# Kernel tuning notes

Measured on AMD Instinct MI355X. Metric: run time of the kernel, lower is better.

Reference implementation:

```python
import jax, jax.numpy as jnp
import numpy as np

B, C, H, W = 4, 256, 64, 64
DQ = C // 8

def setup_inputs() -> dict:
    key = jax.random.key(0)
    ks = jax.random.split(key, 7)
    x = jax.random.normal(ks[0], (B, C, H, W), dtype=jnp.float32)
    # 1x1 convs == per-pixel linear layers: weight [out, in], bias [out]
    Wq = jax.random.normal(ks[1], (DQ, C), dtype=jnp.float32) * (1.0 / np.sqrt(C))
    bq = jax.random.normal(ks[2], (DQ,), dtype=jnp.float32) * 0.01
    Wk = jax.random.normal(ks[3], (DQ, C), dtype=jnp.float32) * (1.0 / np.sqrt(C))
    bk = jax.random.normal(ks[4], (DQ,), dtype=jnp.float32) * 0.01
    Wv = jax.random.normal(ks[5], (C, C), dtype=jnp.float32) * (1.0 / np.sqrt(C))
    bv = jax.random.normal(ks[6], (C,), dtype=jnp.float32) * 0.01
    return {"x": x, "Wq": Wq, "bq": bq, "Wk": Wk, "bk": bk, "Wv": Wv, "bv": bv}

def reference(x, Wq, bq, Wk, bk, Wv, bv):
    b, c, h, w = x.shape
    n = h * w
    xf = x.reshape(b, c, n)                                  # [b,c,n]
    Q = jnp.einsum('dc,bcn->bnd', Wq, xf) + bq               # [b,n,dq]
    K = jnp.einsum('dc,bcn->bdn', Wk, xf) + bk[None, :, None]  # [b,dq,n]
    A = jax.nn.softmax(jnp.einsum('bnd,bdm->bnm', Q, K), axis=-1)  # [b,n,n]
    V = jnp.einsum('oc,bcn->bon', Wv, xf) + bv[None, :, None]      # [b,c,n]
    # torch: bmm(V, A^T) -> out[b,c,i] = sum_j V[b,c,j] * A[b,i,j]
    out = jnp.einsum('bcj,bij->bci', V, A)
    return x + out.reshape(b, c, h, w)
```

## Files before the change

kernel.cpp:

```cpp
#include <hip/hip_runtime.h>
#include <math.h>

#define BB 4
#define CC 256
#define NN 4096
#define DQ 32
#define LOG2E 1.44269504f

typedef _Float16 half8 __attribute__((ext_vector_type(8)));
typedef _Float16 half4 __attribute__((ext_vector_type(4)));
typedef float float4v __attribute__((ext_vector_type(4)));

__global__ __launch_bounds__(64) void prep_kernel(
    const float* __restrict__ Wq, const float* __restrict__ bq,
    const float* __restrict__ Wk, const float* __restrict__ bk,
    const float* __restrict__ Wv, const float* __restrict__ bv,
    _Float16* __restrict__ Wh, float* __restrict__ bh)
{
    int o = blockIdx.x, t = threadIdx.x;
    const float* src; float scale = 1.0f, bias;
    if (o < DQ)            { src = Wq + o * CC;        scale = LOG2E; bias = bq[o] * LOG2E; }
    else if (o < 2 * DQ)   { src = Wk + (o - DQ) * CC;                bias = bk[o - DQ]; }
    else                   { src = Wv + (o - 2 * DQ) * CC;            bias = bv[o - 2 * DQ]; }
    float4 v = *(const float4*)(src + t * 4);
    half4 h = { (_Float16)(v.x * scale), (_Float16)(v.y * scale),
                (_Float16)(v.z * scale), (_Float16)(v.w * scale) };
    *(half4*)(Wh + o * CC + t * 4) = h;
    if (t == 0) bh[o] = bias;
}

__global__ __launch_bounds__(256) void proj_kernel(
    const float* __restrict__ x, const _Float16* __restrict__ Wh,
    const float* __restrict__ bh,
    _Float16* __restrict__ Qt, _Float16* __restrict__ Kt,
    _Float16* __restrict__ Vh)
{
    __shared__ _Float16 xl[64 * 256];
    __shared__ _Float16 os_qk[64 * 72];
    __shared__ _Float16 os_v[256 * 72];

    const int tid = threadIdx.x;
    const int lane = tid & 63, w = tid >> 6;
    const int i16 = lane & 15, q = lane >> 4;
    const int n0 = blockIdx.x * 64, b = blockIdx.y;

    const float* xb = x + (size_t)b * CC * NN + n0;
    #pragma unroll
    for (int u = 0; u < 16; ++u) {
        int idx = u * 256 + tid;
        int c = idx >> 4, n4 = idx & 15;
        float4 v = *(const float4*)(xb + (size_t)c * NN + n4 * 4);
        int chunk = c >> 3, cl = c & 7;
        float vv[4] = {v.x, v.y, v.z, v.w};
        #pragma unroll
        for (int e = 0; e < 4; ++e) {
            int n = n4 * 4 + e;
            xl[n * 256 + ((chunk ^ (n & 31)) * 8) + cl] = (_Float16)vv[e];
        }
    }

    float4v acc[5][4];
    const int obase = 80 * w;
    #pragma unroll
    for (int ot = 0; ot < 5; ++ot) {
        float4 b4 = *(const float4*)(bh + obase + 16 * ot + 4 * q);
        #pragma unroll
        for (int nt = 0; nt < 4; ++nt)
            acc[ot][nt] = (float4v){b4.x, b4.y, b4.z, b4.w};
    }
    __syncthreads();

    #pragma unroll
    for (int k = 0; k < 8; ++k) {
        half8 af[5], bf[4];
        #pragma unroll
        for (int ot = 0; ot < 5; ++ot)
            af[ot] = *(const half8*)(Wh + (size_t)(obase + 16 * ot + i16) * CC + k * 32 + 8 * q);
        #pragma unroll
        for (int nt = 0; nt < 4; ++nt) {
            int n = 16 * nt + i16;
            bf[nt] = *(const half8*)&xl[n * 256 + (((4 * k + q) ^ (n & 31)) * 8)];
        }
        #pragma unroll
        for (int ot = 0; ot < 5; ++ot)
            #pragma unroll
            for (int nt = 0; nt < 4; ++nt)
                acc[ot][nt] = __builtin_amdgcn_mfma_f32_16x16x32_f16(af[ot], bf[nt], acc[ot][nt], 0, 0, 0);
    }

    #pragma unroll
    for (int ot = 0; ot < 5; ++ot) {
        int og = obase + 16 * ot;
        #pragma unroll
        for (int nt = 0; nt < 4; ++nt) {
            int n = 16 * nt + i16;
            if (og < 64) {
                half4 hv = { (_Float16)acc[ot][nt][0], (_Float16)acc[ot][nt][1],
                             (_Float16)acc[ot][nt][2], (_Float16)acc[ot][nt][3] };
                *(half4*)&os_qk[n * 72 + og + 4 * q] = hv;
            } else {
                int cb = og - 64 + 4 * q;
                #pragma unroll
                for (int r = 0; r < 4; ++r)
                    os_v[(cb + r) * 72 + n] = (_Float16)acc[ot][nt][r];
            }
        }
    }
    __syncthreads();

    _Float16* Qtb = Qt + (size_t)b * NN * DQ;
    _Float16* Ktb = Kt + (size_t)b * NN * DQ;
    #pragma unroll
    for (int u = 0; u < 2; ++u) {
        int ct = u * 256 + tid;
        int n = ct >> 3, p = ct & 7;
        half8 hv = *(const half8*)&os_qk[n * 72 + 8 * p];
        if (p < 4) *(half8*)(Qtb + (size_t)(n0 + n) * DQ + 8 * p) = hv;
        else       *(half8*)(Ktb + (size_t)(n0 + n) * DQ + 8 * (p - 4)) = hv;
    }
    _Float16* Vb = Vh + (size_t)b * CC * NN;
    #pragma unroll
    for (int u = 0; u < 8; ++u) {
        int c = u * 32 + (tid >> 3), p = tid & 7;
        half8 hv = *(const half8*)&os_v[c * 72 + 8 * p];
        *(half8*)(Vb + (size_t)c * NN + n0 + 8 * p) = hv;
    }
}

__global__ __launch_bounds__(256) void rowstat_kernel(
    const _Float16* __restrict__ Qt, const _Float16* __restrict__ Kt,
    float* __restrict__ M2, float* __restrict__ L)
{
    __shared__ _Float16 k_lds[64 * 32];
    const int tid = threadIdx.x;
    const int lane = tid & 63, w = tid >> 6;
    const int i16 = lane & 15, q = lane >> 4;
    const int q0 = blockIdx.x * 64, js = blockIdx.y, b = blockIdx.z;

    const _Float16* Qtb = Qt + (size_t)b * NN * DQ;
    const _Float16* Ktb = Kt + (size_t)b * NN * DQ;
    half8 qb = *(const half8*)(Qtb + (size_t)(q0 + 16 * w + i16) * DQ + 8 * q);

    float m = -INFINITY, l = 0.f;
    for (int j0 = js * 2048; j0 < (js + 1) * 2048; j0 += 64) {
        __syncthreads();
        {
            int j = tid >> 2, dg = tid & 3;
            half8 kv = *(const half8*)(Ktb + (size_t)(j0 + j) * DQ + 8 * dg);
            *(half8*)&k_lds[j * 32 + ((dg ^ (j & 3)) * 8)] = kv;
        }
        __syncthreads();
        float4v s[4];
        #pragma unroll
        for (int jt = 0; jt < 4; ++jt) {
            int j = 16 * jt + i16;
            half8 ka = *(const half8*)&k_lds[j * 32 + ((q ^ (j & 3)) * 8)];
            float4v z = {0.f, 0.f, 0.f, 0.f};
            s[jt] = __builtin_amdgcn_mfma_f32_16x16x32_f16(ka, qb, z, 0, 0, 0);
        }
        float tmax = s[0][0];
        #pragma unroll
        for (int jt = 0; jt < 4; ++jt)
            #pragma unroll
            for (int r = 0; r < 4; ++r)
                tmax = fmaxf(tmax, s[jt][r]);
        float mnew = fmaxf(m, tmax);
        float sum = 0.f;
        #pragma unroll
        for (int jt = 0; jt < 4; ++jt)
            #pragma unroll
            for (int r = 0; r < 4; ++r)
                sum += exp2f(s[jt][r] - mnew);
        l = l * exp2f(m - mnew) + sum;
        m = mnew;
    }
    #pragma unroll
    for (int off = 16; off <= 32; off <<= 1) {
        float mo = __shfl_xor(m, off, 64);
        float lo = __shfl_xor(l, off, 64);
        float mn = fmaxf(m, mo);
        l = l * exp2f(m - mn) + lo * exp2f(mo - mn);
        m = mn;
    }
    if (q == 0) {
        int qi = q0 + 16 * w + i16;
        M2[((size_t)b * 2 + js) * NN + qi] = m;
        L[((size_t)b * 2 + js) * NN + qi] = l;
    }
}

__global__ __launch_bounds__(256) void attn_kernel(
    const float* __restrict__ x,
    const _Float16* __restrict__ Qt, const _Float16* __restrict__ Kt,
    const _Float16* __restrict__ Vh,
    const float* __restrict__ M2, const float* __restrict__ L,
    float* __restrict__ out)
{
    __shared__ _Float16 k_lds[64 * 32];
    __shared__ _Float16 v_lds[256 * 64];
    __shared__ _Float16 ps[32 * 72];

    const int tid = threadIdx.x;
    const int w = tid >> 6, lane = tid & 63;
    const int i16 = lane & 15, q = lane >> 4;
    const int i0 = blockIdx.x * 32, b = blockIdx.y;

    const _Float16* Ktb = Kt + (size_t)b * NN * DQ;
    const _Float16* Vb  = Vh + (size_t)b * CC * NN;

    float m2v[2], linv[2];
    #pragma unroll
    for (int it = 0; it < 2; ++it) {
        int qi = i0 + 16 * it + i16;
        float m0 = M2[((size_t)b * 2 + 0) * NN + qi];
        float m1 = M2[((size_t)b * 2 + 1) * NN + qi];
        float l0 = L[((size_t)b * 2 + 0) * NN + qi];
        float l1 = L[((size_t)b * 2 + 1) * NN + qi];
        float mm = fmaxf(m0, m1);
        float ll = l0 * exp2f(m0 - mm) + l1 * exp2f(m1 - mm);
        m2v[it] = mm;
        linv[it] = 1.0f / ll;
    }

    half8 qb[2];
    {
        const _Float16* Qtb = Qt + (size_t)b * NN * DQ;
        qb[0] = *(const half8*)(Qtb + (size_t)(i0 + i16) * DQ + 8 * q);
        qb[1] = *(const half8*)(Qtb + (size_t)(i0 + 16 + i16) * DQ + 8 * q);
    }

    float4v O[4][2];
    #pragma unroll
    for (int ct = 0; ct < 4; ++ct)
        #pragma unroll
        for (int it = 0; it < 2; ++it)
            O[ct][it] = (float4v){0.f, 0.f, 0.f, 0.f};

    for (int j0 = 0; j0 < NN; j0 += 64) {
        __syncthreads();
        {
            int j = tid >> 2, dg = tid & 3;
            half8 kv = *(const half8*)(Ktb + (size_t)(j0 + j) * DQ + 8 * dg);
            *(half8*)&k_lds[j * 32 + ((dg ^ (j & 3)) * 8)] = kv;
        }
        {
            int cb = tid >> 3, jg = tid & 7;
            #pragma unroll
            for (int u = 0; u < 8; ++u) {
                int c = u * 32 + cb;
                half8 vv = *(const half8*)(Vb + (size_t)c * NN + j0 + jg * 8);
                *(half8*)&v_lds[c * 64 + ((jg ^ (c & 7)) * 8)] = vv;
            }
        }
        __syncthreads();

        {
            int j = 16 * w + i16;
            half8 ka = *(const half8*)&k_lds[j * 32 + ((q ^ (j & 3)) * 8)];
            #pragma unroll
            for (int it = 0; it < 2; ++it) {
                float4v z = {0.f, 0.f, 0.f, 0.f};
                float4v s = __builtin_amdgcn_mfma_f32_16x16x32_f16(ka, qb[it], z, 0, 0, 0);
                half4 hv = { (_Float16)exp2f(s[0] - m2v[it]),
                             (_Float16)exp2f(s[1] - m2v[it]),
                             (_Float16)exp2f(s[2] - m2v[it]),
                             (_Float16)exp2f(s[3] - m2v[it]) };
                *(half4*)&ps[(16 * it + i16) * 72 + 16 * w + 4 * q] = hv;
            }
        }
        __syncthreads();

        half8 pb[2][2];
        #pragma unroll
        for (int ks = 0; ks < 2; ++ks)
            #pragma unroll
            for (int it = 0; it < 2; ++it)
                pb[ks][it] = *(const half8*)&ps[(16 * it + i16) * 72 + 32 * ks + 8 * q];
        #pragma unroll
        for (int ct = 0; ct < 4; ++ct) {
            int c = 64 * w + 16 * ct + i16;
            #pragma unroll
            for (int ks = 0; ks < 2; ++ks) {
                int g = 4 * ks + q;
                half8 va = *(const half8*)&v_lds[c * 64 + ((g ^ (c & 7)) * 8)];
                #pragma unroll
                for (int it = 0; it < 2; ++it)
                    O[ct][it] = __builtin_amdgcn_mfma_f32_16x16x32_f16(va, pb[ks][it], O[ct][it], 0, 0, 0);
            }
        }
    }

    const float* xb = x + (size_t)b * CC * NN;
    float* ob = out + (size_t)b * CC * NN;
    #pragma unroll
    for (int ct = 0; ct < 4; ++ct)
        #pragma unroll
        for (int it = 0; it < 2; ++it)
            #pragma unroll
            for (int r = 0; r < 4; ++r) {
                int c = 64 * w + 16 * ct + 4 * q + r;
                size_t idx = (size_t)c * NN + i0 + 16 * it + i16;
                ob[idx] = xb[idx] + O[ct][it][r] * linv[it];
            }
}

extern "C" void kernel_launch(void* const* d_in, const int* in_sizes, int n_in,
                              void* d_out, int out_size, void* d_ws, size_t ws_size,
                              hipStream_t stream) {
    const float* x  = (const float*)d_in[0];
    const float* Wq = (const float*)d_in[1];
    const float* bq = (const float*)d_in[2];
    const float* Wk = (const float*)d_in[3];
    const float* bk = (const float*)d_in[4];
    const float* Wv = (const float*)d_in[5];
    const float* bv = (const float*)d_in[6];
    float* out = (float*)d_out;

    char* ws = (char*)d_ws;
    _Float16* Wh = (_Float16*)(ws);
    float*    bh = (float*)(ws + 163840);
    _Float16* Qt = (_Float16*)(ws + 262144);
    _Float16* Kt = (_Float16*)(ws + 1310720);
    _Float16* Vh = (_Float16*)(ws + 2359296);
    float*    M2 = (float*)(ws + 10747904);
    float*    L  = (float*)(ws + 10878976);

    prep_kernel<<<dim3(320), 64, 0, stream>>>(Wq, bq, Wk, bk, Wv, bv, Wh, bh);
    proj_kernel<<<dim3(NN / 64, BB), 256, 0, stream>>>(x, Wh, bh, Qt, Kt, Vh);
    rowstat_kernel<<<dim3(NN / 64, 2, BB), 256, 0, stream>>>(Qt, Kt, M2, L);
    attn_kernel<<<dim3(NN / 32, BB), 256, 0, stream>>>(x, Qt, Kt, Vh, M2, L, out);
}
```

Before: 205.7 us.

## Split attention over channel halves, prefetch K/V tiles, and widen kernel grids

The attention kernel is split across two channel halves per query tile, which doubles the grid and halves V shared-memory use. K and V tiles for the next iteration are now loaded into registers while the current tile is computed, and MFMA sections are wrapped with s_setprio. The row-stat kernel splits keys four ways and proj_kernel uses 32-pixel tiles, both for more blocks and occupancy. The channel split makes each half recompute QK^T and the exponentials, so that work is doubled.

```diff
diff --git a/kernel.cpp b/kernel.cpp
--- a/kernel.cpp
+++ b/kernel.cpp
@@ -35,56 +35,56 @@
     _Float16* __restrict__ Qt, _Float16* __restrict__ Kt,
     _Float16* __restrict__ Vh)
 {
-    __shared__ _Float16 xl[64 * 256];
-    __shared__ _Float16 os_qk[64 * 72];
-    __shared__ _Float16 os_v[256 * 72];
+    __shared__ _Float16 xl[32 * 256];
+    __shared__ _Float16 os_qk[32 * 72];
+    __shared__ _Float16 os_v[256 * 40];
 
     const int tid = threadIdx.x;
     const int lane = tid & 63, w = tid >> 6;
     const int i16 = lane & 15, q = lane >> 4;
-    const int n0 = blockIdx.x * 64, b = blockIdx.y;
+    const int n0 = blockIdx.x * 32, b = blockIdx.y;
 
     const float* xb = x + (size_t)b * CC * NN + n0;
     #pragma unroll
-    for (int u = 0; u < 16; ++u) {
+    for (int u = 0; u < 8; ++u) {
         int idx = u * 256 + tid;
-        int c = idx >> 4, n4 = idx & 15;
+        int c = idx >> 3, n4 = idx & 7;
         float4 v = *(const float4*)(xb + (size_t)c * NN + n4 * 4);
         int chunk = c >> 3, cl = c & 7;
         float vv[4] = {v.x, v.y, v.z, v.w};
         #pragma unroll
         for (int e = 0; e < 4; ++e) {
             int n = n4 * 4 + e;
-            xl[n * 256 + ((chunk ^ (n & 31)) * 8) + cl] = (_Float16)vv[e];
-        }
-    }
-
-    float4v acc[5][4];
+            xl[n * 256 + ((chunk ^ n) * 8) + cl] = (_Float16)vv[e];
+        }
+    }
+
+    float4v acc[5][2];
     const int obase = 80 * w;
     #pragma unroll
     for (int ot = 0; ot < 5; ++ot) {
         float4 b4 = *(const float4*)(bh + obase + 16 * ot + 4 * q);
         #pragma unroll
-        for (int nt = 0; nt < 4; ++nt)
+        for (int nt = 0; nt < 2; ++nt)
             acc[ot][nt] = (float4v){b4.x, b4.y, b4.z, b4.w};
     }
     __syncthreads();
 
     #pragma unroll
     for (int k = 0; k < 8; ++k) {
-        half8 af[5], bf[4];
+        half8 af[5], bf[2];
         #pragma unroll
         for (int ot = 0; ot < 5; ++ot)
             af[ot] = *(const half8*)(Wh + (size_t)(obase + 16 * ot + i16) * CC + k * 32 + 8 * q);
         #pragma unroll
-        for (int nt = 0; nt < 4; ++nt) {
+        for (int nt = 0; nt < 2; ++nt) {
             int n = 16 * nt + i16;
-            bf[nt] = *(const half8*)&xl[n * 256 + (((4 * k + q) ^ (n & 31)) * 8)];
+            bf[nt] = *(const half8*)&xl[n * 256 + (((4 * k + q) ^ n) * 8)];
         }
         #pragma unroll
         for (int ot = 0; ot < 5; ++ot)
             #pragma unroll
-            for (int nt = 0; nt < 4; ++nt)
+            for (int nt = 0; nt < 2; ++nt)
                 acc[ot][nt] = __builtin_amdgcn_mfma_f32_16x16x32_f16(af[ot], bf[nt], acc[ot][nt], 0, 0, 0);
     }
 
@@ -92,7 +92,7 @@
     for (int ot = 0; ot < 5; ++ot) {
         int og = obase + 16 * ot;
         #pragma unroll
-        for (int nt = 0; nt < 4; ++nt) {
+        for (int nt = 0; nt < 2; ++nt) {
             int n = 16 * nt + i16;
             if (og < 64) {
                 half4 hv = { (_Float16)acc[ot][nt][0], (_Float16)acc[ot][nt][1],
@@ -102,7 +102,7 @@
                 int cb = og - 64 + 4 * q;
                 #pragma unroll
                 for (int r = 0; r < 4; ++r)
-                    os_v[(cb + r) * 72 + n] = (_Float16)acc[ot][nt][r];
+                    os_v[(cb + r) * 40 + n] = (_Float16)acc[ot][nt][r];
             }
         }
     }
@@ -110,19 +110,17 @@
 
     _Float16* Qtb = Qt + (size_t)b * NN * DQ;
     _Float16* Ktb = Kt + (size_t)b * NN * DQ;
-    #pragma unroll
-    for (int u = 0; u < 2; ++u) {
-        int ct = u * 256 + tid;
-        int n = ct >> 3, p = ct & 7;
+    {
+        int n = tid >> 3, p = tid & 7;
         half8 hv = *(const half8*)&os_qk[n * 72 + 8 * p];
         if (p < 4) *(half8*)(Qtb + (size_t)(n0 + n) * DQ + 8 * p) = hv;
         else       *(half8*)(Ktb + (size_t)(n0 + n) * DQ + 8 * (p - 4)) = hv;
     }
     _Float16* Vb = Vh + (size_t)b * CC * NN;
     #pragma unroll
-    for (int u = 0; u < 8; ++u) {
-        int c = u * 32 + (tid >> 3), p = tid & 7;
-        half8 hv = *(const half8*)&os_v[c * 72 + 8 * p];
+    for (int u = 0; u < 4; ++u) {
+        int c = u * 64 + (tid >> 2), p = tid & 3;
+        half8 hv = *(const half8*)&os_v[c * 40 + 8 * p];
         *(half8*)(Vb + (size_t)c * NN + n0 + 8 * p) = hv;
     }
 }
@@ -141,16 +139,19 @@
     const _Float16* Ktb = Kt + (size_t)b * NN * DQ;
     half8 qb = *(const half8*)(Qtb + (size_t)(q0 + 16 * w + i16) * DQ + 8 * q);
 
+    const int jb = js * 1024;
+    const int jl = tid >> 2, dg = tid & 3;
+    half8 kv = *(const half8*)(Ktb + (size_t)(jb + jl) * DQ + 8 * dg);
+
     float m = -INFINITY, l = 0.f;
-    for (int j0 = js * 2048; j0 < (js + 1) * 2048; j0 += 64) {
-        __syncthreads();
-        {
-            int j = tid >> 2, dg = tid & 3;
-            half8 kv = *(const half8*)(Ktb + (size_t)(j0 + j) * DQ + 8 * dg);
-            *(half8*)&k_lds[j * 32 + ((dg ^ (j & 3)) * 8)] = kv;
-        }
-        __syncthreads();
+    for (int t = 0; t < 16; ++t) {
+        __syncthreads();
+        *(half8*)&k_lds[jl * 32 + ((dg ^ (jl & 3)) * 8)] = kv;
+        __syncthreads();
+        if (t < 15)
+            kv = *(const half8*)(Ktb + (size_t)(jb + (t + 1) * 64 + jl) * DQ + 8 * dg);
         float4v s[4];
+        __builtin_amdgcn_s_setprio(1);
         #pragma unroll
         for (int jt = 0; jt < 4; ++jt) {
             int j = 16 * jt + i16;
@@ -158,6 +159,7 @@
             float4v z = {0.f, 0.f, 0.f, 0.f};
             s[jt] = __builtin_amdgcn_mfma_f32_16x16x32_f16(ka, qb, z, 0, 0, 0);
         }
+        __builtin_amdgcn_s_setprio(0);
         float tmax = s[0][0];
         #pragma unroll
         for (int jt = 0; jt < 4; ++jt)
@@ -184,8 +186,8 @@
     }
     if (q == 0) {
         int qi = q0 + 16 * w + i16;
-        M2[((size_t)b * 2 + js) * NN + qi] = m;
-        L[((size_t)b * 2 + js) * NN + qi] = l;
+        M2[((size_t)b * 4 + js) * NN + qi] = m;
+        L[((size_t)b * 4 + js) * NN + qi] = l;
     }
 }
 
@@ -197,27 +199,31 @@
     float* __restrict__ out)
 {
     __shared__ _Float16 k_lds[64 * 32];
-    __shared__ _Float16 v_lds[256 * 64];
+    __shared__ _Float16 v_lds[128 * 64];
     __shared__ _Float16 ps[32 * 72];
 
     const int tid = threadIdx.x;
     const int w = tid >> 6, lane = tid & 63;
     const int i16 = lane & 15, q = lane >> 4;
-    const int i0 = blockIdx.x * 32, b = blockIdx.y;
+    const int i0 = blockIdx.x * 32, cs = blockIdx.y, b = blockIdx.z;
+    const int c0 = cs * 128;
 
     const _Float16* Ktb = Kt + (size_t)b * NN * DQ;
-    const _Float16* Vb  = Vh + (size_t)b * CC * NN;
+    const _Float16* Vb  = Vh + (size_t)b * CC * NN + (size_t)c0 * NN;
 
     float m2v[2], linv[2];
     #pragma unroll
     for (int it = 0; it < 2; ++it) {
         int qi = i0 + 16 * it + i16;
-        float m0 = M2[((size_t)b * 2 + 0) * NN + qi];
-        float m1 = M2[((size_t)b * 2 + 1) * NN + qi];
-        float l0 = L[((size_t)b * 2 + 0) * NN + qi];
-        float l1 = L[((size_t)b * 2 + 1) * NN + qi];
-        float mm = fmaxf(m0, m1);
-        float ll = l0 * exp2f(m0 - mm) + l1 * exp2f(m1 - mm);
+        float mm = -INFINITY, ll = 0.f;
+        #pragma unroll
+        for (int p = 0; p < 4; ++p) {
+            float mp = M2[((size_t)b * 4 + p) * NN + qi];
+            float lp = L [((size_t)b * 4 + p) * NN + qi];
+            float mn = fmaxf(mm, mp);
+            ll = ll * exp2f(mm - mn) + lp * exp2f(mp - mn);
+            mm = mn;
+        }
         m2v[it] = mm;
         linv[it] = 1.0f / ll;
     }
@@ -229,30 +235,38 @@
         qb[1] = *(const half8*)(Qtb + (size_t)(i0 + 16 + i16) * DQ + 8 * q);
     }
 
-    float4v O[4][2];
-    #pragma unroll
-    for (int ct = 0; ct < 4; ++ct)
+    float4v O[2][2];
+    #pragma unroll
+    for (int ct = 0; ct < 2; ++ct)
         #pragma unroll
         for (int it = 0; it < 2; ++it)
             O[ct][it] = (float4v){0.f, 0.f, 0.f, 0.f};
 
+    const int jK = tid >> 2, dgK = tid & 3;
+    const int cbV = tid >> 3, jgV = tid & 7;
+
+    half8 kv, vv[4];
+    kv = *(const half8*)(Ktb + (size_t)jK * DQ + 8 * dgK);
+    #pragma unroll
+    for (int u = 0; u < 4; ++u)
+        vv[u] = *(const half8*)(Vb + (size_t)(u * 32 + cbV) * NN + 8 * jgV);
+
     for (int j0 = 0; j0 < NN; j0 += 64) {
         __syncthreads();
-        {
-            int j = tid >> 2, dg = tid & 3;
-            half8 kv = *(const half8*)(Ktb + (size_t)(j0 + j) * DQ + 8 * dg);
-            *(half8*)&k_lds[j * 32 + ((dg ^ (j & 3)) * 8)] = kv;
-        }
-        {
-            int cb = tid >> 3, jg = tid & 7;
-            #pragma unroll
-            for (int u = 0; u < 8; ++u) {
-                int c = u * 32 + cb;
-                half8 vv = *(const half8*)(Vb + (size_t)c * NN + j0 + jg * 8);
-                *(half8*)&v_lds[c * 64 + ((jg ^ (c & 7)) * 8)] = vv;
-            }
-        }
-        __syncthreads();
+        *(half8*)&k_lds[jK * 32 + ((dgK ^ (jK & 3)) * 8)] = kv;
+        #pragma unroll
+        for (int u = 0; u < 4; ++u) {
+            int c = u * 32 + cbV;
+            *(half8*)&v_lds[c * 64 + ((jgV ^ (c & 7)) * 8)] = vv[u];
+        }
+        __syncthreads();
+
+        if (j0 + 64 < NN) {
+            kv = *(const half8*)(Ktb + (size_t)(j0 + 64 + jK) * DQ + 8 * dgK);
+            #pragma unroll
+            for (int u = 0; u < 4; ++u)
+                vv[u] = *(const half8*)(Vb + (size_t)(u * 32 + cbV) * NN + (j0 + 64) + 8 * jgV);
+        }
 
         {
             int j = 16 * w + i16;
@@ -276,9 +290,10 @@
             #pragma unroll
             for (int it = 0; it < 2; ++it)
                 pb[ks][it] = *(const half8*)&ps[(16 * it + i16) * 72 + 32 * ks + 8 * q];
-        #pragma unroll
-        for (int ct = 0; ct < 4; ++ct) {
-            int c = 64 * w + 16 * ct + i16;
+        __builtin_amdgcn_s_setprio(1);
+        #pragma unroll
+        for (int ct = 0; ct < 2; ++ct) {
+            int c = 32 * w + 16 * ct + i16;
             #pragma unroll
             for (int ks = 0; ks < 2; ++ks) {
                 int g = 4 * ks + q;
@@ -288,17 +303,18 @@
                     O[ct][it] = __builtin_amdgcn_mfma_f32_16x16x32_f16(va, pb[ks][it], O[ct][it], 0, 0, 0);
             }
         }
+        __builtin_amdgcn_s_setprio(0);
     }
 
     const float* xb = x + (size_t)b * CC * NN;
     float* ob = out + (size_t)b * CC * NN;
     #pragma unroll
-    for (int ct = 0; ct < 4; ++ct)
+    for (int ct = 0; ct < 2; ++ct)
         #pragma unroll
         for (int it = 0; it < 2; ++it)
             #pragma unroll
             for (int r = 0; r < 4; ++r) {
-                int c = 64 * w + 16 * ct + 4 * q + r;
+                int c = c0 + 32 * w + 16 * ct + 4 * q + r;
                 size_t idx = (size_t)c * NN + i0 + 16 * it + i16;
                 ob[idx] = xb[idx] + O[ct][it][r] * linv[it];
             }
@@ -323,10 +339,10 @@
     _Float16* Kt = (_Float16*)(ws + 1310720);
     _Float16* Vh = (_Float16*)(ws + 2359296);
     float*    M2 = (float*)(ws + 10747904);
-    float*    L  = (float*)(ws + 10878976);
+    float*    L  = (float*)(ws + 11010048);
 
     prep_kernel<<<dim3(320), 64, 0, stream>>>(Wq, bq, Wk, bk, Wv, bv, Wh, bh);
-    proj_kernel<<<dim3(NN / 64, BB), 256, 0, stream>>>(x, Wh, bh, Qt, Kt, Vh);
-    rowstat_kernel<<<dim3(NN / 64, 2, BB), 256, 0, stream>>>(Qt, Kt, M2, L);
-    attn_kernel<<<dim3(NN / 32, BB), 256, 0, stream>>>(x, Qt, Kt, Vh, M2, L, out);
-}
+    proj_kernel<<<dim3(NN / 32, BB), 256, 0, stream>>>(x, Wh, bh, Qt, Kt, Vh);
+    rowstat_kernel<<<dim3(NN / 64, 4, BB), 256, 0, stream>>>(Qt, Kt, M2, L);
+    attn_kernel<<<dim3(NN / 32, 2, BB), 256, 0, stream>>>(x, Qt, Kt, Vh, M2, L, out);
+}
```

New measurement: 202.5 us. Within noise of the previous version (-1.5%).
